# Kernel optimization log

Measured on AMD Instinct MI355X. Metric: run time of the kernel, lower is better.

Reference implementation:

```python
import jax, jax.numpy as jnp
import numpy as np

HEADS = 8
EPS = 1e-5

def _conv_bn_gelu(x, w, b, g, beta):
    # x: (B, Cin, L), w: (Cout, Cin, 3), stride 2, padding 1
    y = jax.lax.conv_general_dilated(x, w, (2,), [(1, 1)],
                                     dimension_numbers=('NCH', 'OIH', 'NCH'))
    y = y + b[None, :, None]
    # BatchNorm1d in training mode: stats over (batch, length) per channel
    m = y.mean((0, 2), keepdims=True)
    v = ((y - m) ** 2).mean((0, 2), keepdims=True)
    y = g[None, :, None] * (y - m) * jax.lax.rsqrt(v + EPS) + beta[None, :, None]
    return jax.nn.gelu(y, approximate=False)  # torch nn.GELU default = exact erf

def _ln(x, g, b):
    m = x.mean(-1, keepdims=True)
    v = ((x - m) ** 2).mean(-1, keepdims=True)
    return (x - m) * jax.lax.rsqrt(v + EPS) * g + b

def _block(x, wq, wk, wv, wo, w1, b1, w2, b2, l1g, l1b, l2g, l2b):
    B, S, E = x.shape
    hd = E // HEADS
    q = (x @ wq.T).reshape(B, S, HEADS, hd).transpose(0, 2, 1, 3)  # bhsd
    k = (x @ wk.T).reshape(B, S, HEADS, hd).transpose(0, 2, 1, 3)
    v = (x @ wv.T).reshape(B, S, HEADS, hd).transpose(0, 2, 1, 3)
    energy = jnp.einsum('bhqd,bhkd->bhqk', q, k) / (hd ** 0.5)
    attn = jax.nn.softmax(energy, axis=-1)
    o = jnp.einsum('bhqk,bhkd->bhqd', attn, v).transpose(0, 2, 1, 3).reshape(B, S, E)
    o = o @ wo.T
    h = _ln(o + x, l1g, l1b)
    f = jnp.maximum(h @ w1.T + b1, 0.0) @ w2.T + b2
    return _ln(f + h, l2g, l2b)

def setup_inputs() -> dict:
    key = jax.random.key(0)
    keys = iter(jax.random.split(key, 64))
    def nrm(shape, s=0.02):
        return jax.random.normal(next(keys), shape, jnp.float32) * s
    d = {"x": jax.random.normal(next(keys), (32, 14, 8192), jnp.float32)}
    chans = [(14, 512), (512, 512), (512, 512), (512, 512), (512, 1536)]
    for i, (ci, co) in enumerate(chans):
        d[f"cw{i}"] = nrm((co, ci, 3))
        d[f"cb{i}"] = jnp.zeros((co,), jnp.float32)
        d[f"g{i}"] = jnp.ones((co,), jnp.float32)
        d[f"be{i}"] = jnp.zeros((co,), jnp.float32)
    L, E, F = 8, 1536, 3076
    for n in ["wq", "wk", "wv", "wo"]:
        d[n] = nrm((L, E, E))
    d["w1"] = nrm((L, F, E)); d["b1"] = jnp.zeros((L, F), jnp.float32)
    d["w2"] = nrm((L, E, F)); d["b2"] = jnp.zeros((L, E), jnp.float32)
    d["ln1g"] = jnp.ones((L, E), jnp.float32); d["ln1b"] = jnp.zeros((L, E), jnp.float32)
    d["ln2g"] = jnp.ones((L, E), jnp.float32); d["ln2b"] = jnp.zeros((L, E), jnp.float32)
    return d

def reference(x, cw0, cb0, g0, be0, cw1, cb1, g1, be1, cw2, cb2, g2, be2,
              cw3, cb3, g3, be3, cw4, cb4, g4, be4,
              wq, wk, wv, wo, w1, b1, w2, b2, ln1g, ln1b, ln2g, ln2b):
    for cw, cb, g, be in [(cw0, cb0, g0, be0), (cw1, cb1, g1, be1),
                          (cw2, cb2, g2, be2), (cw3, cb3, g3, be3),
                          (cw4, cb4, g4, be4)]:
        x = _conv_bn_gelu(x, cw, cb, g, be)
    x = jnp.transpose(x, (0, 2, 1))  # (B, S, E)
    for i in range(wq.shape[0]):
        x = _block(x, wq[i], wk[i], wv[i], wo[i], w1[i], b1[i], w2[i], b2[i],
                   ln1g[i], ln1b[i], ln2g[i], ln2b[i])
    return x
```

## Files before the change

kernel.cpp:

```cpp
#include <hip/hip_runtime.h>
#include <hip/hip_bf16.h>
#include <math.h>

using bf16 = __hip_bfloat16;
typedef float f32x4 __attribute__((ext_vector_type(4)));
typedef short mfrag __attribute__((ext_vector_type(8)));

#define DEVI __device__ __forceinline__

DEVI void gll16(const void* g, void* l) {
  __builtin_amdgcn_global_load_lds(
      (const __attribute__((address_space(1))) void*)g,
      (__attribute__((address_space(3))) void*)l, 16, 0, 0);
}

enum { EPI_F32 = 0, EPI_BF16 = 1, EPI_RELU = 2, EPI_RES = 3, EPI_QKV = 4, EPI_OSC = 5 };

struct GArgs {
  const bf16* A; const bf16* B;
  float* Cf; bf16* Cb;
  long sA, sB, sC;
  int K, lda, ldb, ldc;
  float scale;
  const float* bias; const float* res;
  int LoutShift, Lin; const bf16* zp;
  bf16 *q, *k, *vt, *o;
};

template <int EPI, bool GATHER>
__global__ __launch_bounds__(256) void gemm_k(GArgs p) {
  __shared__ alignas(16) bf16 As[128 * 32];
  __shared__ alignas(16) bf16 Bs[128 * 32];
  const int tid = threadIdx.x;
  const int wave = tid >> 6, lane = tid & 63;

  const int nx = gridDim.x, ny = gridDim.y;
  int bid = blockIdx.x + nx * blockIdx.y;
  int band = bid / (nx * 8);
  int rem = bid - band * nx * 8;
  int bh = ny - band * 8; if (bh > 8) bh = 8;
  int nt = rem / bh, mt = band * 8 + (rem - nt * bh);
  const int m0 = mt * 128, n0 = nt * 128;

  const long zb = blockIdx.z;
  const bf16* Ab = p.A + zb * p.sA;
  const bf16* Bb = p.B + zb * p.sB;
  const int sr = tid >> 2;
  const int scol = (((tid & 3) ^ ((sr >> 1) & 3)) * 8);
  const int wr = wave >> 1, wcl = wave & 1;
  const int qd = lane >> 4, r16 = lane & 15;
  const int rg = (qd ^ ((r16 >> 1) & 3)) * 8;
  char* AsB = (char*)As + wave * 1024;
  char* BsB = (char*)Bs + wave * 1024;

  f32x4 acc[4][4] = {};

  for (int k0 = 0; k0 < p.K; k0 += 32) {
    const bf16 *ga0, *ga1;
    if (GATHER) {
      const int kk = k0 + scol;
      const int tap = kk >> 9, ci = kk & 511;
      const int LoutM = (1 << p.LoutShift) - 1;
      int m1 = m0 + sr;
      int l1 = m1 & LoutM, b1 = m1 >> p.LoutShift;
      int lin1 = 2 * l1 + tap - 1;
      ga0 = ((unsigned)lin1 < (unsigned)p.Lin)
                ? Ab + (((long)(b1 * p.Lin + lin1)) << 9) + ci : p.zp;
      int m2 = m0 + 64 + sr;
      int l2 = m2 & LoutM, b2 = m2 >> p.LoutShift;
      int lin2 = 2 * l2 + tap - 1;
      ga1 = ((unsigned)lin2 < (unsigned)p.Lin)
                ? Ab + (((long)(b2 * p.Lin + lin2)) << 9) + ci : p.zp;
    } else {
      ga0 = Ab + (long)(m0 + sr) * p.lda + k0 + scol;
      ga1 = Ab + (long)(m0 + 64 + sr) * p.lda + k0 + scol;
    }
    const bf16* gb0 = Bb + (long)(n0 + sr) * p.ldb + k0 + scol;
    const bf16* gb1 = Bb + (long)(n0 + 64 + sr) * p.ldb + k0 + scol;
    gll16(ga0, AsB);
    gll16(ga1, AsB + 4096);
    gll16(gb0, BsB);
    gll16(gb1, BsB + 4096);
    __syncthreads();

    mfrag af[4], bfv[4];
#pragma unroll
    for (int i = 0; i < 4; i++)
      af[i] = *(const mfrag*)&As[(wr * 64 + i * 16 + r16) * 32 + rg];
#pragma unroll
    for (int j = 0; j < 4; j++)
      bfv[j] = *(const mfrag*)&Bs[(wcl * 64 + j * 16 + r16) * 32 + rg];
#pragma unroll
    for (int i = 0; i < 4; i++)
#pragma unroll
      for (int j = 0; j < 4; j++)
        acc[i][j] = __builtin_amdgcn_mfma_f32_16x16x32_bf16(af[i], bfv[j], acc[i][j], 0, 0, 0);
    __syncthreads();
  }

  const int erow = m0 + wr * 64 + qd * 4;
#pragma unroll
  for (int j = 0; j < 4; j++) {
    const int gn = n0 + wcl * 64 + j * 16 + r16;
    if constexpr (EPI == EPI_OSC) { if (gn >= 192) continue; }
    float bias_v = 0.f;
    if constexpr (EPI == EPI_RELU) bias_v = p.bias[gn];
    if constexpr (EPI == EPI_RES)  bias_v = p.bias ? p.bias[gn] : 0.f;
    bf16* qkv_base = nullptr; long qkv_coff = 0; int seg = 0;
    if constexpr (EPI == EPI_QKV) {
      int nn;
      if (gn < 1536)      { qkv_base = p.q;  nn = gn; }
      else if (gn < 3072) { qkv_base = p.k;  nn = gn - 1536; }
      else                { qkv_base = p.vt; nn = gn - 3072; seg = 1; }
      const int h = nn / 192, d = nn - h * 192;
      qkv_coff = seg ? ((long)h * 65536 + (long)d * 256)
                     : ((long)h * 49152 + d);
    }
#pragma unroll
    for (int i = 0; i < 4; i++) {
#pragma unroll
      for (int v = 0; v < 4; v++) {
        const int gm = erow + i * 16 + v;
        float val = acc[i][j][v] * p.scale;
        if constexpr (EPI == EPI_F32) {
          p.Cf[zb * p.sC + (long)gm * p.ldc + gn] = val;
        } else if constexpr (EPI == EPI_BF16) {
          p.Cb[(long)gm * p.ldc + gn] = (bf16)val;
        } else if constexpr (EPI == EPI_RELU) {
          p.Cb[(long)gm * p.ldc + gn] = (bf16)fmaxf(val + bias_v, 0.f);
        } else if constexpr (EPI == EPI_RES) {
          const long idx = (long)gm * p.ldc + gn;
          p.Cf[idx] = val + bias_v + p.res[idx];
        } else if constexpr (EPI == EPI_QKV) {
          const int bq = gm >> 8, s = gm & 255;
          const long idx = seg ? (qkv_coff + (long)bq * 524288 + s)
                               : (qkv_coff + (long)bq * 393216 + (long)s * 192);
          qkv_base[idx] = (bf16)val;
        } else if constexpr (EPI == EPI_OSC) {
          const int bq = (int)(zb >> 3), h = (int)(zb & 7);
          p.o[((long)bq * 256 + gm) * 1536 + h * 192 + gn] = (bf16)val;
        }
      }
    }
  }
}

__global__ __launch_bounds__(256) void conv0_k(const float* __restrict__ x,
                                               const float* __restrict__ w, bf16* Y) {
  const int b = blockIdx.y, l0 = blockIdx.x * 16;
  __shared__ float xs[14 * 33];
  const int t = threadIdx.x;
  for (int i = t; i < 14 * 33; i += 256) {
    int ci = i / 33, pp = i - ci * 33;
    int pos = 2 * l0 - 1 + pp;
    xs[i] = (pos >= 0 && pos < 8192) ? x[((long)b * 14 + ci) * 8192 + pos] : 0.f;
  }
  float wr0[42], wr1[42];
  const int co0 = 2 * t;
#pragma unroll
  for (int i = 0; i < 42; i++) { wr0[i] = w[co0 * 42 + i]; wr1[i] = w[co0 * 42 + 42 + i]; }
  __syncthreads();
  for (int l = 0; l < 16; l++) {
    float a0 = 0.f, a1 = 0.f;
#pragma unroll
    for (int ci = 0; ci < 14; ci++)
#pragma unroll
      for (int k = 0; k < 3; k++) {
        float xv = xs[ci * 33 + 2 * l + k];
        a0 += xv * wr0[ci * 3 + k];
        a1 += xv * wr1[ci * 3 + k];
      }
    long orow = ((long)b * 4096 + l0 + l) * 512;
    Y[orow + co0] = (bf16)a0;
    Y[orow + co0 + 1] = (bf16)a1;
  }
}

__global__ void bn_stats_k(const bf16* __restrict__ Y, float* stats, int rows, int C) {
  const int c = blockIdx.x * 256 + threadIdx.x;
  const int rpb = rows / gridDim.y;
  const int r0 = blockIdx.y * rpb;
  float s = 0.f, ss = 0.f;
  const bf16* p = Y + (long)r0 * C + c;
  for (int r = 0; r < rpb; ++r) { float v = (float)(*p); s += v; ss += v * v; p += C; }
  atomicAdd(&stats[2 * c], s);
  atomicAdd(&stats[2 * c + 1], ss);
}

__global__ void bn_gelu_k(const bf16* __restrict__ Y, const float* __restrict__ stats,
                          const float* __restrict__ g, const float* __restrict__ be,
                          bf16* outB, float* outF, long n, int C, float invN) {
  long i = blockIdx.x * 256L + threadIdx.x;
  const long st = (long)gridDim.x * 256;
  for (; i < n; i += st) {
    int c = (int)(i % C);
    float m = stats[2 * c] * invN;
    float var = stats[2 * c + 1] * invN - m * m;
    float rs = rsqrtf(fmaxf(var, 0.f) + 1e-5f);
    float xn = ((float)Y[i] - m) * rs * g[c] + be[c];
    float ge = 0.5f * xn * (1.f + erff(xn * 0.70710678118f));
    outB[i] = (bf16)ge;
    if (outF) outF[i] = ge;
  }
}

__global__ __launch_bounds__(256) void ln_k(const float* __restrict__ in,
                                            const float* __restrict__ g,
                                            const float* __restrict__ b,
                                            float* outF, bf16* outB) {
  const int row = blockIdx.x, t = threadIdx.x;
  const float* r = in + (long)row * 1536;
  float v[6]; float s = 0.f;
#pragma unroll
  for (int i = 0; i < 6; i++) { v[i] = r[t + 256 * i]; s += v[i]; }
  __shared__ float red[256];
  red[t] = s; __syncthreads();
#pragma unroll
  for (int o = 128; o > 0; o >>= 1) { if (t < o) red[t] += red[t + o]; __syncthreads(); }
  const float mean = red[0] * (1.f / 1536.f);
  __syncthreads();
  float ss = 0.f;
#pragma unroll
  for (int i = 0; i < 6; i++) { float d = v[i] - mean; ss += d * d; }
  red[t] = ss; __syncthreads();
#pragma unroll
  for (int o = 128; o > 0; o >>= 1) { if (t < o) red[t] += red[t + o]; __syncthreads(); }
  const float rstd = rsqrtf(red[0] * (1.f / 1536.f) + 1e-5f);
#pragma unroll
  for (int i = 0; i < 6; i++) {
    int c = t + 256 * i;
    float o_ = (v[i] - mean) * rstd * g[c] + b[c];
    if (outF) outF[(long)row * 1536 + c] = o_;
    if (outB) outB[(long)row * 1536 + c] = (bf16)o_;
  }
}

__global__ void softmax_k(const float* __restrict__ sc, bf16* P) {
  const int row = blockIdx.x * 4 + (threadIdx.x >> 6);
  const int lane = threadIdx.x & 63;
  const float* r = sc + (long)row * 256;
  float v0 = r[lane], v1 = r[lane + 64], v2 = r[lane + 128], v3 = r[lane + 192];
  float mx = fmaxf(fmaxf(v0, v1), fmaxf(v2, v3));
  for (int m = 32; m > 0; m >>= 1) mx = fmaxf(mx, __shfl_xor(mx, m));
  v0 = expf(v0 - mx); v1 = expf(v1 - mx); v2 = expf(v2 - mx); v3 = expf(v3 - mx);
  float s = v0 + v1 + v2 + v3;
  for (int m = 32; m > 0; m >>= 1) s += __shfl_xor(s, m);
  const float inv = 1.f / s;
  bf16* o = P + (long)row * 256;
  o[lane] = (bf16)(v0 * inv); o[lane + 64] = (bf16)(v1 * inv);
  o[lane + 128] = (bf16)(v2 * inv); o[lane + 192] = (bf16)(v3 * inv);
}

__global__ void zero_k(float* p, int n) {
  int i = blockIdx.x * 256 + threadIdx.x;
  if (i < n) p[i] = 0.f;
}

__global__ void pack_qkv_k(const float* wq, const float* wk, const float* wv, bf16* out) {
  const int c = blockIdx.x * 256 + threadIdx.x;
  const int r = blockIdx.y;
  const float* src; int rr;
  if (r < 1536) { src = wq; rr = r; }
  else if (r < 3072) { src = wk; rr = r - 1536; }
  else { src = wv; rr = r - 3072; }
  out[(long)r * 1536 + c] = (bf16)src[(long)rr * 1536 + c];
}

__global__ void cast_k(const float* in, bf16* out, long n) {
  long i = blockIdx.x * 256L + threadIdx.x;
  const long st = (long)gridDim.x * 256;
  for (; i < n; i += st) out[i] = (bf16)in[i];
}

__global__ void pack_w1_k(const float* w1, bf16* out) {
  const int c = blockIdx.x * 256 + threadIdx.x;
  const int r = blockIdx.y;
  float v = (r < 3076) ? w1[(long)r * 1536 + c] : 0.f;
  out[(long)r * 1536 + c] = (bf16)v;
}

__global__ void pack_w2_k(const float* w2, bf16* out) {
  const int c = blockIdx.x * 128 + threadIdx.x;
  const int r = blockIdx.y;
  float v = (c < 3076) ? w2[(long)r * 3076 + c] : 0.f;
  out[(long)r * 3200 + c] = (bf16)v;
}

__global__ void pack_b1_k(const float* b1, float* out) {
  const int c = blockIdx.x * 128 + threadIdx.x;
  const int l = blockIdx.y;
  out[l * 3200 + c] = (c < 3076) ? b1[l * 3076 + c] : 0.f;
}

__global__ void pack_conv_k(const float* w, bf16* out) {
  const int co = blockIdx.x;
  for (int i = threadIdx.x; i < 1536; i += 256) {
    int k = i >> 9, ci = i & 511;
    out[(long)co * 1536 + i] = (bf16)w[(co * 512 + ci) * 3 + k];
  }
}

extern "C" void kernel_launch(void* const* d_in, const int* in_sizes, int n_in,
                              void* d_out, int out_size, void* d_ws, size_t ws_size,
                              hipStream_t stream) {
  const float* x_in = (const float*)d_in[0];
  const float *cw[5], *gg[5], *bb[5];
  for (int i = 0; i < 5; i++) {
    cw[i] = (const float*)d_in[1 + 4 * i];
    gg[i] = (const float*)d_in[3 + 4 * i];
    bb[i] = (const float*)d_in[4 + 4 * i];
  }
  const float* wq = (const float*)d_in[21];
  const float* wk = (const float*)d_in[22];
  const float* wv = (const float*)d_in[23];
  const float* wo = (const float*)d_in[24];
  const float* w1 = (const float*)d_in[25];
  const float* b1 = (const float*)d_in[26];
  const float* w2 = (const float*)d_in[27];
  const float* b2 = (const float*)d_in[28];
  const float* ln1g = (const float*)d_in[29];
  const float* ln1b = (const float*)d_in[30];
  const float* ln2g = (const float*)d_in[31];
  const float* ln2b = (const float*)d_in[32];

  char* ws = (char*)d_ws;
  size_t off = 0;
  auto alloc = [&](size_t bytes) -> char* {
    off = (off + 255) & ~(size_t)255;
    char* p = ws + off; off += bytes; return p;
  };
  bf16* zp = (bf16*)alloc(256);
  float* stats = (float*)alloc(3072 * 4);
  float* b1p = (float*)alloc(8L * 3200 * 4);
  bf16* wqkv_l = (bf16*)alloc(4608L * 1536 * 2);
  bf16* wo_l   = (bf16*)alloc(1536L * 1536 * 2);
  bf16* w1_l   = (bf16*)alloc(3200L * 1536 * 2);
  bf16* w2_l   = (bf16*)alloc(1536L * 3200 * 2);
  bf16* wconv  = (bf16*)alloc(1536L * 1536 * 2);
  char* A = alloc(134217728);
  char* Bq = alloc(67108864);
  bf16* xb = (bf16*)alloc(8192L * 1536 * 2);
  float* xf = (float*)d_out;

  bf16*  vtb    = (bf16*)A;
  float* scores = (float*)(A + 33554432);
  bf16*  P      = (bf16*)(A + 100663296);
  bf16*  qb     = (bf16*)Bq;
  bf16*  kb     = (bf16*)(Bq + 25165824);
  bf16*  ob     = (bf16*)Bq;
  float* rf  = (float*)A;
  bf16*  hb  = (bf16*)(A + 50331648);
  bf16*  mid = (bf16*)(A + 75497472);
  float* hf  = (float*)Bq;
  bf16* cY0 = (bf16*)A;
  bf16* cY1 = (bf16*)Bq;
  bf16* cY2 = (bf16*)A;
  bf16* cY3 = (bf16*)Bq;
  bf16* cY4 = (bf16*)A;

  zero_k<<<1, 256, 0, stream>>>((float*)zp, 64);
  pack_b1_k<<<dim3(25, 8), 128, 0, stream>>>(b1, b1p);

  conv0_k<<<dim3(256, 32), 256, 0, stream>>>(x_in, cw[0], cY0);

  auto bn = [&](const bf16* Y, bf16* outB, float* outF, int rows, int C,
                const float* g_, const float* be_) {
    zero_k<<<12, 256, 0, stream>>>(stats, 3072);
    bn_stats_k<<<dim3(C / 256, 256), 256, 0, stream>>>(Y, stats, rows, C);
    bn_gelu_k<<<4096, 256, 0, stream>>>(Y, stats, g_, be_, outB, outF,
                                        (long)rows * C, C, 1.f / (float)rows);
  };
  auto conv_gemm = [&](const bf16* Gin, const float* wsrc, int Cout, bf16* Yout,
                       int M, int N, int LoutShift, int Lin) {
    pack_conv_k<<<Cout, 256, 0, stream>>>(wsrc, wconv);
    GArgs a{}; a.A = Gin; a.B = wconv; a.Cb = Yout;
    a.K = 1536; a.ldb = 1536; a.ldc = N; a.scale = 1.f;
    a.LoutShift = LoutShift; a.Lin = Lin; a.zp = zp;
    gemm_k<EPI_BF16, true><<<dim3(N / 128, M / 128, 1), 256, 0, stream>>>(a);
  };

  bn(cY0, cY0, nullptr, 131072, 512, gg[0], bb[0]);
  conv_gemm(cY0, cw[1], 512, cY1, 65536, 512, 11, 4096);
  bn(cY1, cY1, nullptr, 65536, 512, gg[1], bb[1]);
  conv_gemm(cY1, cw[2], 512, cY2, 32768, 512, 10, 2048);
  bn(cY2, cY2, nullptr, 32768, 512, gg[2], bb[2]);
  conv_gemm(cY2, cw[3], 512, cY3, 16384, 512, 9, 1024);
  bn(cY3, cY3, nullptr, 16384, 512, gg[3], bb[3]);
  conv_gemm(cY3, cw[4], 1536, cY4, 8192, 1536, 8, 512);
  bn(cY4, xb, xf, 8192, 1536, gg[4], bb[4]);

  for (int l = 0; l < 8; l++) {
    pack_qkv_k<<<dim3(6, 4608), 256, 0, stream>>>(wq + (long)l * 1536 * 1536,
                                                  wk + (long)l * 1536 * 1536,
                                                  wv + (long)l * 1536 * 1536, wqkv_l);
    cast_k<<<2048, 256, 0, stream>>>(wo + (long)l * 1536 * 1536, wo_l, 1536L * 1536);
    pack_w1_k<<<dim3(6, 3200), 256, 0, stream>>>(w1 + (long)l * 3076 * 1536, w1_l);
    pack_w2_k<<<dim3(25, 1536), 128, 0, stream>>>(w2 + (long)l * 1536 * 3076, w2_l);

    {
      GArgs a{}; a.A = xb; a.B = wqkv_l;
      a.K = 1536; a.lda = 1536; a.ldb = 1536; a.scale = 1.f;
      a.q = qb; a.k = kb; a.vt = vtb;
      gemm_k<EPI_QKV, false><<<dim3(36, 64, 1), 256, 0, stream>>>(a);
    }
    {
      GArgs a{}; a.A = qb; a.B = kb; a.Cf = scores;
      a.sA = 49152; a.sB = 49152; a.sC = 65536;
      a.K = 192; a.lda = 192; a.ldb = 192; a.ldc = 256;
      a.scale = 0.07216878364870323f;
      gemm_k<EPI_F32, false><<<dim3(2, 2, 256), 256, 0, stream>>>(a);
    }
    softmax_k<<<16384, 256, 0, stream>>>(scores, P);
    {
      GArgs a{}; a.A = P; a.B = vtb; a.sA = 65536; a.sB = 65536;
      a.K = 256; a.lda = 256; a.ldb = 256; a.scale = 1.f; a.o = ob;
      gemm_k<EPI_OSC, false><<<dim3(2, 2, 256), 256, 0, stream>>>(a);
    }
    {
      GArgs a{}; a.A = ob; a.B = wo_l; a.Cf = rf;
      a.K = 1536; a.lda = 1536; a.ldb = 1536; a.ldc = 1536; a.scale = 1.f;
      a.bias = nullptr; a.res = xf;
      gemm_k<EPI_RES, false><<<dim3(12, 64, 1), 256, 0, stream>>>(a);
    }
    ln_k<<<8192, 256, 0, stream>>>(rf, ln1g + l * 1536, ln1b + l * 1536, hf, hb);
    {
      GArgs a{}; a.A = hb; a.B = w1_l; a.Cb = mid;
      a.K = 1536; a.lda = 1536; a.ldb = 1536; a.ldc = 3200; a.scale = 1.f;
      a.bias = b1p + l * 3200;
      gemm_k<EPI_RELU, false><<<dim3(25, 64, 1), 256, 0, stream>>>(a);
    }
    {
      GArgs a{}; a.A = mid; a.B = w2_l; a.Cf = rf;
      a.K = 3200; a.lda = 3200; a.ldb = 3200; a.ldc = 1536; a.scale = 1.f;
      a.bias = b2 + l * 1536; a.res = hf;
      gemm_k<EPI_RES, false><<<dim3(12, 64, 1), 256, 0, stream>>>(a);
    }
    if (l < 7)
      ln_k<<<8192, 256, 0, stream>>>(rf, ln2g + l * 1536, ln2b + l * 1536, xf, xb);
    else
      ln_k<<<8192, 256, 0, stream>>>(rf, ln2g + l * 1536, ln2b + l * 1536,
                                     (float*)d_out, nullptr);
  }
}
```

Before: 7.964 ms.

## Add 256x256 tile GEMM kernel with LDS double buffering and XCD-aware scheduling

```diff
diff --git a/kernel.cpp b/kernel.cpp
--- a/kernel.cpp
+++ b/kernel.cpp
@@ -13,6 +13,14 @@
       (const __attribute__((address_space(1))) void*)g,
       (__attribute__((address_space(3))) void*)l, 16, 0, 0);
 }
+
+DEVI void barx() {
+  __builtin_amdgcn_s_barrier();
+  __builtin_amdgcn_sched_barrier(0);
+}
+#define LGKM0() asm volatile("s_waitcnt lgkmcnt(0)" ::: "memory")
+#define VMCNT2() asm volatile("s_waitcnt vmcnt(2)" ::: "memory")
+#define VMCNT0() asm volatile("s_waitcnt vmcnt(0)" ::: "memory")
 
 enum { EPI_F32 = 0, EPI_BF16 = 1, EPI_RELU = 2, EPI_RES = 3, EPI_QKV = 4, EPI_OSC = 5 };
 
@@ -26,6 +34,205 @@
   int LoutShift, Lin; const bf16* zp;
   bf16 *q, *k, *vt, *o;
 };
+
+template <int EPI, bool GATHER>
+__global__ __launch_bounds__(512, 2) void gemm256_k(GArgs p) {
+  __shared__ char sm[131072];
+  const int tid = threadIdx.x;
+  const int wave = tid >> 6, lane = tid & 63;
+  const int wm = wave >> 2, wn = wave & 3;
+  const int qd = lane >> 4, r16 = lane & 15;
+
+  const int ntN = gridDim.x;
+  const int total = ntN * gridDim.y;
+  const int bid = blockIdx.x + ntN * blockIdx.y;
+  const int q8 = total >> 3, r8 = total & 7;
+  const int xcd = bid & 7, idx = bid >> 3;
+  const int wg = (xcd < r8 ? xcd * (q8 + 1) : r8 * (q8 + 1) + (xcd - r8) * q8) + idx;
+  const int mt = wg / ntN, nt = wg - mt * ntN;
+  const int m0 = mt * 256, n0 = nt * 256;
+
+  const bf16* Ab = p.A;
+  const bf16* Bb = p.B;
+
+  const int rowt = tid >> 3;
+  const int slot = tid & 7;
+  const int cs8 = (slot ^ (rowt & 7)) * 8;
+  const int woff = wave * 1024;
+
+  auto stA = [&](char* dstA, int c, int k) {
+    const bf16* s;
+    if constexpr (GATHER) {
+      const int row = m0 + c * 64 + rowt;
+      const int col = k + cs8;
+      const int LoutM = (1 << p.LoutShift) - 1;
+      const int l = row & LoutM, b = row >> p.LoutShift;
+      const int tap = col >> 9, ci = col & 511;
+      const int lin = 2 * l + tap - 1;
+      s = ((unsigned)lin < (unsigned)p.Lin)
+              ? Ab + (((long)(b * p.Lin + lin)) << 9) + ci : p.zp;
+    } else {
+      s = Ab + (long)(m0 + c * 64 + rowt) * p.lda + k + cs8;
+    }
+    gll16(s, dstA + c * 8192 + woff);
+  };
+  auto stB = [&](char* dstB, int c, int k) {
+    gll16(Bb + (long)(n0 + c * 64 + rowt) * p.ldb + k + cs8, dstB + c * 8192 + woff);
+  };
+
+  const int xw = (r16 & 7) << 4;
+  const int c0 = (qd * 16) ^ xw;
+  const int c1 = (qd * 16 + 64) ^ xw;
+  const int rbA = (wm * 128 + r16) * 128;
+  const int rbB = 32768 + (wn * 64 + r16) * 128;
+
+  f32x4 acc[8][4] = {};
+  const int NT = p.K >> 6;
+
+  {
+    char* dA = sm;
+    char* dB = sm + 32768;
+    stB(dB, 0, 0); stB(dB, 1, 0); stB(dB, 2, 0); stB(dB, 3, 0);
+    stA(dA, 0, 0); stA(dA, 2, 0); stA(dA, 1, 0); stA(dA, 3, 0);
+  }
+  VMCNT2();
+  barx();
+
+  for (int t = 0; t < NT; ++t) {
+    char* bc = sm + (t & 1) * 65536;
+    char* bnA = sm + ((t & 1) ^ 1) * 65536;
+    char* bnB = bnA + 32768;
+    const int k1 = (t + 1) << 6;
+    const bool notlast = (t + 1 < NT);
+
+    mfrag af[4], bf[4];
+
+    {
+      const char* aB = bc + rbA;
+      af[0] = *(const mfrag*)(aB + 0 * 2048 + c0);
+      af[1] = *(const mfrag*)(aB + 1 * 2048 + c0);
+      af[2] = *(const mfrag*)(aB + 2 * 2048 + c0);
+      af[3] = *(const mfrag*)(aB + 3 * 2048 + c0);
+      const char* bB = bc + rbB;
+      bf[0] = *(const mfrag*)(bB + 0 * 2048 + c0);
+      bf[1] = *(const mfrag*)(bB + 1 * 2048 + c0);
+      bf[2] = *(const mfrag*)(bB + 2 * 2048 + c0);
+      bf[3] = *(const mfrag*)(bB + 3 * 2048 + c0);
+      if (notlast) { stB(bnB, 0, k1); stB(bnB, 1, k1); }
+      barx();
+      __builtin_amdgcn_s_setprio(1);
+#pragma unroll
+      for (int i2 = 0; i2 < 4; i2++)
+#pragma unroll
+        for (int j = 0; j < 4; j++)
+          acc[i2][j] = __builtin_amdgcn_mfma_f32_16x16x32_bf16(af[i2], bf[j], acc[i2][j], 0, 0, 0);
+      __builtin_amdgcn_s_setprio(0);
+      LGKM0();
+      if (notlast) VMCNT2(); else VMCNT0();
+      barx();
+    }
+    {
+      const char* aB = bc + rbA + 8192;
+      af[0] = *(const mfrag*)(aB + 0 * 2048 + c0);
+      af[1] = *(const mfrag*)(aB + 1 * 2048 + c0);
+      af[2] = *(const mfrag*)(aB + 2 * 2048 + c0);
+      af[3] = *(const mfrag*)(aB + 3 * 2048 + c0);
+      if (notlast) { stB(bnB, 2, k1); stB(bnB, 3, k1); }
+      barx();
+      __builtin_amdgcn_s_setprio(1);
+#pragma unroll
+      for (int i2 = 0; i2 < 4; i2++)
+#pragma unroll
+        for (int j = 0; j < 4; j++)
+          acc[4 + i2][j] = __builtin_amdgcn_mfma_f32_16x16x32_bf16(af[i2], bf[j], acc[4 + i2][j], 0, 0, 0);
+      __builtin_amdgcn_s_setprio(0);
+      LGKM0();
+      barx();
+    }
+    {
+      const char* aB = bc + rbA;
+      af[0] = *(const mfrag*)(aB + 0 * 2048 + c1);
+      af[1] = *(const mfrag*)(aB + 1 * 2048 + c1);
+      af[2] = *(const mfrag*)(aB + 2 * 2048 + c1);
+      af[3] = *(const mfrag*)(aB + 3 * 2048 + c1);
+      const char* bB = bc + rbB;
+      bf[0] = *(const mfrag*)(bB + 0 * 2048 + c1);
+      bf[1] = *(const mfrag*)(bB + 1 * 2048 + c1);
+      bf[2] = *(const mfrag*)(bB + 2 * 2048 + c1);
+      bf[3] = *(const mfrag*)(bB + 3 * 2048 + c1);
+      if (notlast) { stA(bnA, 0, k1); stA(bnA, 2, k1); }
+      barx();
+      __builtin_amdgcn_s_setprio(1);
+#pragma unroll
+      for (int i2 = 0; i2 < 4; i2++)
+#pragma unroll
+        for (int j = 0; j < 4; j++)
+          acc[i2][j] = __builtin_amdgcn_mfma_f32_16x16x32_bf16(af[i2], bf[j], acc[i2][j], 0, 0, 0);
+      __builtin_amdgcn_s_setprio(0);
+      LGKM0();
+      barx();
+    }
+    {
+      const char* aB = bc + rbA + 8192;
+      af[0] = *(const mfrag*)(aB + 0 * 2048 + c1);
+      af[1] = *(const mfrag*)(aB + 1 * 2048 + c1);
+      af[2] = *(const mfrag*)(aB + 2 * 2048 + c1);
+      af[3] = *(const mfrag*)(aB + 3 * 2048 + c1);
+      if (notlast) { stA(bnA, 1, k1); stA(bnA, 3, k1); }
+      barx();
+      __builtin_amdgcn_s_setprio(1);
+#pragma unroll
+      for (int i2 = 0; i2 < 4; i2++)
+#pragma unroll
+        for (int j = 0; j < 4; j++)
+          acc[4 + i2][j] = __builtin_amdgcn_mfma_f32_16x16x32_bf16(af[i2], bf[j], acc[4 + i2][j], 0, 0, 0);
+      __builtin_amdgcn_s_setprio(0);
+      LGKM0();
+      if (notlast) VMCNT2();
+      barx();
+    }
+  }
+
+  const int erow = m0 + wm * 128 + qd * 4;
+#pragma unroll
+  for (int j = 0; j < 4; j++) {
+    const int gn = n0 + wn * 64 + j * 16 + r16;
+    float bias_v = 0.f;
+    if constexpr (EPI == EPI_RELU) bias_v = p.bias[gn];
+    if constexpr (EPI == EPI_RES)  bias_v = p.bias ? p.bias[gn] : 0.f;
+    bf16* qkv_base = nullptr; long qkv_coff = 0; int seg = 0;
+    if constexpr (EPI == EPI_QKV) {
+      int nn;
+      if (gn < 1536)      { qkv_base = p.q;  nn = gn; }
+      else if (gn < 3072) { qkv_base = p.k;  nn = gn - 1536; }
+      else                { qkv_base = p.vt; nn = gn - 3072; seg = 1; }
+      const int h = nn / 192, d = nn - h * 192;
+      qkv_coff = seg ? ((long)h * 65536 + (long)d * 256)
+                     : ((long)h * 49152 + d);
+    }
+#pragma unroll
+    for (int i = 0; i < 8; i++) {
+#pragma unroll
+      for (int v = 0; v < 4; v++) {
+        const int gm = erow + i * 16 + v;
+        float val = acc[i][j][v] * p.scale;
+        if constexpr (EPI == EPI_BF16) {
+          p.Cb[(long)gm * p.ldc + gn] = (bf16)val;
+        } else if constexpr (EPI == EPI_RELU) {
+          p.Cb[(long)gm * p.ldc + gn] = (bf16)fmaxf(val + bias_v, 0.f);
+        } else if constexpr (EPI == EPI_RES) {
+          const long idx = (long)gm * p.ldc + gn;
+          p.Cf[idx] = val + bias_v + p.res[idx];
+        } else if constexpr (EPI == EPI_QKV) {
+          const int bq = gm >> 8, s = gm & 255;
+          const long idx = seg ? (qkv_coff + (long)bq * 524288 + s)
+                               : (qkv_coff + (long)bq * 393216 + (long)s * 192);
+          qkv_base[idx] = (bf16)val;
+        }
+      }
+    }
+  }
+}
 
 template <int EPI, bool GATHER>
 __global__ __launch_bounds__(256) void gemm_k(GArgs p) {
@@ -103,19 +310,6 @@
   for (int j = 0; j < 4; j++) {
     const int gn = n0 + wcl * 64 + j * 16 + r16;
     if constexpr (EPI == EPI_OSC) { if (gn >= 192) continue; }
-    float bias_v = 0.f;
-    if constexpr (EPI == EPI_RELU) bias_v = p.bias[gn];
-    if constexpr (EPI == EPI_RES)  bias_v = p.bias ? p.bias[gn] : 0.f;
-    bf16* qkv_base = nullptr; long qkv_coff = 0; int seg = 0;
-    if constexpr (EPI == EPI_QKV) {
-      int nn;
-      if (gn < 1536)      { qkv_base = p.q;  nn = gn; }
-      else if (gn < 3072) { qkv_base = p.k;  nn = gn - 1536; }
-      else                { qkv_base = p.vt; nn = gn - 3072; seg = 1; }
-      const int h = nn / 192, d = nn - h * 192;
-      qkv_coff = seg ? ((long)h * 65536 + (long)d * 256)
-                     : ((long)h * 49152 + d);
-    }
 #pragma unroll
     for (int i = 0; i < 4; i++) {
 #pragma unroll
@@ -124,18 +318,6 @@
         float val = acc[i][j][v] * p.scale;
         if constexpr (EPI == EPI_F32) {
           p.Cf[zb * p.sC + (long)gm * p.ldc + gn] = val;
-        } else if constexpr (EPI == EPI_BF16) {
-          p.Cb[(long)gm * p.ldc + gn] = (bf16)val;
-        } else if constexpr (EPI == EPI_RELU) {
-          p.Cb[(long)gm * p.ldc + gn] = (bf16)fmaxf(val + bias_v, 0.f);
-        } else if constexpr (EPI == EPI_RES) {
-          const long idx = (long)gm * p.ldc + gn;
-          p.Cf[idx] = val + bias_v + p.res[idx];
-        } else if constexpr (EPI == EPI_QKV) {
-          const int bq = gm >> 8, s = gm & 255;
-          const long idx = seg ? (qkv_coff + (long)bq * 524288 + s)
-                               : (qkv_coff + (long)bq * 393216 + (long)s * 192);
-          qkv_base[idx] = (bf16)val;
         } else if constexpr (EPI == EPI_OSC) {
           const int bq = (int)(zb >> 3), h = (int)(zb & 7);
           p.o[((long)bq * 256 + gm) * 1536 + h * 192 + gn] = (bf16)val;
@@ -283,13 +465,13 @@
   const int c = blockIdx.x * 128 + threadIdx.x;
   const int r = blockIdx.y;
   float v = (c < 3076) ? w2[(long)r * 3076 + c] : 0.f;
-  out[(long)r * 3200 + c] = (bf16)v;
+  out[(long)r * 3328 + c] = (bf16)v;
 }
 
 __global__ void pack_b1_k(const float* b1, float* out) {
   const int c = blockIdx.x * 128 + threadIdx.x;
   const int l = blockIdx.y;
-  out[l * 3200 + c] = (c < 3076) ? b1[l * 3076 + c] : 0.f;
+  out[l * 3328 + c] = (c < 3076) ? b1[l * 3076 + c] : 0.f;
 }
 
 __global__ void pack_conv_k(const float* w, bf16* out) {
@@ -331,11 +513,11 @@
   };
   bf16* zp = (bf16*)alloc(256);
   float* stats = (float*)alloc(3072 * 4);
-  float* b1p = (float*)alloc(8L * 3200 * 4);
+  float* b1p = (float*)alloc(8L * 3328 * 4);
   bf16* wqkv_l = (bf16*)alloc(4608L * 1536 * 2);
   bf16* wo_l   = (bf16*)alloc(1536L * 1536 * 2);
-  bf16* w1_l   = (bf16*)alloc(3200L * 1536 * 2);
-  bf16* w2_l   = (bf16*)alloc(1536L * 3200 * 2);
+  bf16* w1_l   = (bf16*)alloc(3328L * 1536 * 2);
+  bf16* w2_l   = (bf16*)alloc(1536L * 3328 * 2);
   bf16* wconv  = (bf16*)alloc(1536L * 1536 * 2);
   char* A = alloc(134217728);
   char* Bq = alloc(67108864);
@@ -359,7 +541,7 @@
   bf16* cY4 = (bf16*)A;
 
   zero_k<<<1, 256, 0, stream>>>((float*)zp, 64);
-  pack_b1_k<<<dim3(25, 8), 128, 0, stream>>>(b1, b1p);
+  pack_b1_k<<<dim3(26, 8), 128, 0, stream>>>(b1, b1p);
 
   conv0_k<<<dim3(256, 32), 256, 0, stream>>>(x_in, cw[0], cY0);
 
@@ -376,7 +558,7 @@
     GArgs a{}; a.A = Gin; a.B = wconv; a.Cb = Yout;
     a.K = 1536; a.ldb = 1536; a.ldc = N; a.scale = 1.f;
     a.LoutShift = LoutShift; a.Lin = Lin; a.zp = zp;
-    gemm_k<EPI_BF16, true><<<dim3(N / 128, M / 128, 1), 256, 0, stream>>>(a);
+    gemm256_k<EPI_BF16, true><<<dim3(N / 256, M / 256, 1), 512, 0, stream>>>(a);
   };
 
   bn(cY0, cY0, nullptr, 131072, 512, gg[0], bb[0]);
@@ -394,14 +576,14 @@
                                                   wk + (long)l * 1536 * 1536,
                                                   wv + (long)l * 1536 * 1536, wqkv_l);
     cast_k<<<2048, 256, 0, stream>>>(wo + (long)l * 1536 * 1536, wo_l, 1536L * 1536);
-    pack_w1_k<<<dim3(6, 3200), 256, 0, stream>>>(w1 + (long)l * 3076 * 1536, w1_l);
-    pack_w2_k<<<dim3(25, 1536), 128, 0, stream>>>(w2 + (long)l * 1536 * 3076, w2_l);
+    pack_w1_k<<<dim3(6, 3328), 256, 0, stream>>>(w1 + (long)l * 3076 * 1536, w1_l);
+    pack_w2_k<<<dim3(26, 1536), 128, 0, stream>>>(w2 + (long)l * 1536 * 3076, w2_l);
 
     {
       GArgs a{}; a.A = xb; a.B = wqkv_l;
       a.K = 1536; a.lda = 1536; a.ldb = 1536; a.scale = 1.f;
       a.q = qb; a.k = kb; a.vt = vtb;
-      gemm_k<EPI_QKV, false><<<dim3(36, 64, 1), 256, 0, stream>>>(a);
+      gemm256_k<EPI_QKV, false><<<dim3(18, 32, 1), 512, 0, stream>>>(a);
     }
     {
       GArgs a{}; a.A = qb; a.B = kb; a.Cf = scores;
@@ -420,20 +602,20 @@
       GArgs a{}; a.A = ob; a.B = wo_l; a.Cf = rf;
       a.K = 1536; a.lda = 1536; a.ldb = 1536; a.ldc = 1536; a.scale = 1.f;
       a.bias = nullptr; a.res = xf;
-      gemm_k<EPI_RES, false><<<dim3(12, 64, 1), 256, 0, stream>>>(a);
+      gemm256_k<EPI_RES, false><<<dim3(6, 32, 1), 512, 0, stream>>>(a);
     }
     ln_k<<<8192, 256, 0, stream>>>(rf, ln1g + l * 1536, ln1b + l * 1536, hf, hb);
     {
       GArgs a{}; a.A = hb; a.B = w1_l; a.Cb = mid;
-      a.K = 1536; a.lda = 1536; a.ldb = 1536; a.ldc = 3200; a.scale = 1.f;
-      a.bias = b1p + l * 3200;
-      gemm_k<EPI_RELU, false><<<dim3(25, 64, 1), 256, 0, stream>>>(a);
+      a.K = 1536; a.lda = 1536; a.ldb = 1536; a.ldc = 3328; a.scale = 1.f;
+      a.bias = b1p + l * 3328;
+      gemm256_k<EPI_RELU, false><<<dim3(13, 32, 1), 512, 0, stream>>>(a);
     }
     {
       GArgs a{}; a.A = mid; a.B = w2_l; a.Cf = rf;
-      a.K = 3200; a.lda = 3200; a.ldb = 3200; a.ldc = 1536; a.scale = 1.f;
+      a.K = 3328; a.lda = 3328; a.ldb = 3328; a.ldc = 1536; a.scale = 1.f;
       a.bias = b2 + l * 1536; a.res = hf;
-      gemm_k<EPI_RES, false><<<dim3(12, 64, 1), 256, 0, stream>>>(a);
+      gemm256_k<EPI_RES, false><<<dim3(6, 32, 1), 512, 0, stream>>>(a);
     }
     if (l < 7)
       ln_k<<<8192, 256, 0, stream>>>(rf, ln2g + l * 1536, ln2b + l * 1536, xf, xb);
```

Measured after the change: 6.754 ms. 15.2% less time.
